# Kernel tuning notes

Measured on AMD Instinct MI355X. Metric: run time of the kernel, lower is better.

The kernel has to match this reference:

```python
import jax, jax.numpy as jnp
import numpy as np

HID = 512
T_CONST = 0.01


def setup_inputs() -> dict:
    key = jax.random.key(0)
    ks = jax.random.split(key, 14)
    B, T, I, H = 32, 1000, 1, HID
    inp = jax.random.normal(ks[0], (B, T, I), jnp.float32)
    hn = jax.random.uniform(ks[1], (1, B, 4 * H), jnp.float32)  # post-relu state, nonneg
    inhib_stim = 0.01 * jax.random.normal(ks[2], (B, T, 4 * H), jnp.float32)
    u = lambda k: jax.random.uniform(k, (H, H), jnp.float32, 0.0, 0.01)
    str2str_w = u(ks[3]); thal2alm_w = u(ks[4]); thal2str_w = u(ks[5])
    alm2alm_w = u(ks[6]); alm2str_w = u(ks[7]); str2snr_w = u(ks[8]); snr2thal_w = u(ks[9])
    inp_weight = jax.random.uniform(ks[10], (I, 4 * H), jnp.float32, 0.0, 0.01)
    sparse_mask = (jax.random.uniform(ks[11], (H, H)) < 0.1).astype(jnp.float32)
    str2str_fixed = jax.random.uniform(ks[12], (H, H), jnp.float32, 0.0, 0.001) * sparse_mask
    return dict(inp=inp, hn=hn, inhib_stim=inhib_stim,
                str2str_w=str2str_w, thal2alm_w=thal2alm_w, thal2str_w=thal2str_w,
                alm2alm_w=alm2alm_w, alm2str_w=alm2str_w, str2snr_w=str2snr_w,
                snr2thal_w=snr2thal_w, inp_weight=inp_weight, str2str_fixed=str2str_fixed)


def reference(inp, hn, inhib_stim, str2str_w, thal2alm_w, thal2str_w,
              alm2alm_w, alm2str_w, str2snr_w, snr2thal_w, inp_weight, str2str_fixed):
    H = str2str_w.shape[0]
    k = int(0.3 * H)  # inhibitory fraction of ALM
    dt = jnp.asarray(T_CONST, inp.dtype)
    ht = lambda w: jnp.clip(w, 1e-15, 1.0)  # F.hardtanh(w, 1e-15, 1)
    Z = jnp.zeros((H, H), inp.dtype)

    # constrained weight blocks (str2str_mask is all zeros, so only the fixed sparse part survives; @ (-I) flips sign)
    str2str = -(0.0 * ht(str2str_w) + str2str_fixed)
    str2snr = -ht(str2snr_w)            # @ (-I)
    snr2thal = -ht(snr2thal_w)          # @ (-I)
    d_alm = jnp.concatenate([jnp.ones(H - k, inp.dtype), -jnp.ones(k, inp.dtype)])
    alm2alm = ht(alm2alm_w) * d_alm[None, :]  # column-scale == @ diag(d_alm)
    alm2str_mask = jnp.concatenate([jnp.ones((H, H - k), inp.dtype), jnp.zeros((H, k), inp.dtype)], axis=1)
    alm2str = alm2str_mask * ht(alm2str_w)
    thal2str_mask = jnp.concatenate([jnp.zeros((H // 2, H), inp.dtype), jnp.ones((H // 2, H), inp.dtype)], axis=0)
    thal2str = thal2str_mask * ht(thal2str_w)
    thal2alm = ht(thal2alm_w)
    iw = ht(inp_weight)

    W_rec = jnp.block([[str2str, Z,        thal2str, alm2str],
                       [str2snr, Z,        Z,        Z      ],
                       [Z,       snr2thal, Z,        Z      ],
                       [Z,       Z,        thal2alm, alm2alm]])  # [4H, 4H]

    strthal_mask = jnp.concatenate([jnp.zeros(H // 2, inp.dtype), jnp.ones(H // 2, inp.dtype),
                                    jnp.zeros(3 * H, inp.dtype)])
    tonic = jnp.concatenate([jnp.zeros(H, inp.dtype), 0.7 * jnp.ones(H, inp.dtype),
                             jnp.ones(H, inp.dtype), jnp.zeros(H, inp.dtype)])

    # precompute time-varying drive (noise=False path): input proj + inhib stim + tonic  [B,T,4H]
    drive = jnp.einsum('bti,ih->bth', inp, iw) * strthal_mask + inhib_stim + tonic

    def step(h, d_t):  # h: [B,4H], d_t: [B,4H]
        h_new = jax.nn.relu(h + dt * (-h + h @ W_rec.T + d_t))
        return h_new, h_new

    h0 = hn[0]  # squeeze(0)
    _, hs = jax.lax.scan(step, h0, jnp.swapaxes(drive, 0, 1))  # hs: [T,B,4H]
    rnn_out = jnp.swapaxes(hs, 0, 1)  # [B,T,4H]
    hn_last = rnn_out[:, -1, :][None]  # [1,B,4H]
    return hn_last, rnn_out
```

## Files before the change

### kernel.cpp

```cpp
#include <hip/hip_runtime.h>
#include <stdint.h>

#define H4T 2048
#define BATCHN 32
#define TSTEPS 1000
#define NBLK 256
#define NTHR 512
#define NSLICE 16
#define WSTRIDE 8192


__device__ __forceinline__ float ht_clip(float w) {
  return fminf(fmaxf(w, 1e-15f), 1.0f);
}

__device__ float wval(int g, int jj, int i,
                      const float* s2s_f, const float* t2s, const float* a2s,
                      const float* s2n, const float* n2t,
                      const float* t2a, const float* a2a) {
  int ig = i >> 9;
  int ii = i & 511;
  float v = 0.0f;
  if (g == 0) {
    if (ig == 0)      v = -s2s_f[jj * 512 + ii];
    else if (ig == 2) v = (jj >= 256) ? ht_clip(t2s[jj * 512 + ii]) : 0.0f;
    else if (ig == 3) v = (ii < 359) ? ht_clip(a2s[jj * 512 + ii]) : 0.0f;
  } else if (g == 1) {
    if (ig == 0)      v = -ht_clip(s2n[jj * 512 + ii]);
  } else if (g == 2) {
    if (ig == 1)      v = -ht_clip(n2t[jj * 512 + ii]);
  } else {
    if (ig == 2)      v = ht_clip(t2a[jj * 512 + ii]);
    else if (ig == 3) v = ht_clip(a2a[jj * 512 + ii]) * ((ii < 359) ? 1.0f : -1.0f);
  }
  return v;
}

__global__ void prep_h0(const float* __restrict__ hn, float* __restrict__ hbuf0) {
  int e = blockIdx.x * blockDim.x + threadIdx.x;
  if (e < BATCHN * H4T) {
    int b = e >> 11;
    int j = e & 2047;
    hbuf0[(j >> 2) * 128 + (b << 2) + (j & 3)] = hn[e];
  }
}

__global__ __launch_bounds__(NTHR) void pack_w(
    const float* s2s_f, const float* t2s, const float* a2s,
    const float* s2n, const float* n2t, const float* t2a, const float* a2a,
    const float* __restrict__ inpw,
    float* __restrict__ wp, float* __restrict__ iwp)
{
  int bid = blockIdx.x, tid = threadIdx.x;
  int g, j0, NC, IE, ib4;
  if (bid < 128)      { g = 0; j0 = bid * 4;              NC = 4;  IE = 1536; ib4 = 0;   }
  else if (bid < 160) { g = 1; j0 = 512 + (bid - 128)*16; NC = 16; IE = 512;  ib4 = 0;   }
  else if (bid < 192) { g = 2; j0 = 1024 + (bid - 160)*16;NC = 16; IE = 512;  ib4 = 128; }
  else                { g = 3; j0 = 1536 + (bid - 192)*8; NC = 8;  IE = 1024; ib4 = 256; }

  for (int idx = tid; idx < NC * IE; idx += NTHR) {
    int c  = idx / IE;
    int fi = idx - c * IE;
    int i  = (g == 0) ? ((fi < 512) ? fi : fi + 512) : ib4 * 4 + fi;
    wp[(size_t)bid * WSTRIDE + idx] =
        wval(g, (j0 + c) & 511, i, s2s_f, t2s, a2s, s2n, n2t, t2a, a2a);
  }
  if (tid < NC) {
    int j = j0 + tid;
    iwp[bid * 16 + tid] = (j >= 256 && j < 512) ? ht_clip(inpw[j]) : 0.0f;
  }
}

template<int NCOLS, int IEXT, bool SPLIT, int LOG2NC>
__device__ __forceinline__ void step_group(
    int j0, int ibase4, float tonicv, int t,
    const float* __restrict__ inp, const float* __restrict__ inhib,
    const float* __restrict__ wp_blk, const float* __restrict__ iwp_blk,
    float* __restrict__ out_hn, float* __restrict__ out_rnn,
    const float* __restrict__ hb, float* __restrict__ hbn,
    float* Wl, float* red, float* outb, float* iwl)
{
  const int tid = threadIdx.x;
  const int b   = tid & 31;
  const int jl  = tid >> 5;
  constexpr int IEXT4  = IEXT / 4;
  constexpr int SLICE4 = IEXT4 / NSLICE;

  {
    const float4* __restrict__ wsrc = (const float4*)wp_blk;
    float4* Wl4w = (float4*)Wl;
    for (int k = tid; k < NCOLS * IEXT4; k += NTHR) Wl4w[k] = wsrc[k];
  }
  if (tid < NCOLS) iwl[tid] = iwp_blk[tid];
  __syncthreads();

  const float dtc = 0.01f;
  const float4* __restrict__ hb4 = (const float4*)hb;
  const float4* __restrict__ Wl4 = (const float4*)Wl;

  float acc[NCOLS];
#pragma unroll
  for (int c = 0; c < NCOLS; ++c) acc[c] = 0.0f;

  for (int it = 0; it < SLICE4; ++it) {
    int fi4 = jl * SLICE4 + it;
    int i4  = ibase4 + (SPLIT ? ((fi4 >= 128) ? fi4 + 128 : fi4) : fi4);
    float4 hv = hb4[i4 * 32 + b];
#pragma unroll
    for (int c = 0; c < NCOLS; ++c) {
      float4 wv = Wl4[c * IEXT4 + fi4];
      acc[c] = fmaf(hv.x, wv.x, acc[c]);
      acc[c] = fmaf(hv.y, wv.y, acc[c]);
      acc[c] = fmaf(hv.z, wv.z, acc[c]);
      acc[c] = fmaf(hv.w, wv.w, acc[c]);
    }
  }

#pragma unroll
  for (int c = 0; c < NCOLS; ++c)
    red[(c * NSLICE + jl) * 33 + b] = acc[c];
  __syncthreads();

  if (tid < 32 * NCOLS) {
    int pb = tid & 31;
    int c  = tid >> 5;
    float s = 0.0f;
#pragma unroll
    for (int sl = 0; sl < NSLICE; ++sl)
      s += red[(c * NSLICE + sl) * 33 + pb];
    int j = j0 + c;
    float hold = hb[(j >> 2) * 128 + (pb << 2) + (j & 3)];
    float inh  = inhib[(size_t)pb * (TSTEPS * H4T) + (size_t)t * H4T + j];
    float iv   = inp[pb * TSTEPS + t];
    float d    = inh + tonicv + iv * iwl[c];
    float hnew = fmaxf(0.0f, fmaf(dtc, s + d - hold, hold));
    hbn[(j >> 2) * 128 + (pb << 2) + (j & 3)] = hnew;
    outb[pb * (NCOLS + 1) + c] = hnew;
  }
  __syncthreads();

  if (tid < 32 * NCOLS) {
    int c  = tid & (NCOLS - 1);
    int bb = tid >> LOG2NC;
    float v = outb[bb * (NCOLS + 1) + c];
    out_rnn[(size_t)bb * (TSTEPS * H4T) + (size_t)t * H4T + (j0 + c)] = v;
    if (t == TSTEPS - 1) out_hn[bb * H4T + (j0 + c)] = v;
  }
}

__global__ __launch_bounds__(NTHR) void rnn_step(
    int t,
    const float* __restrict__ inp, const float* __restrict__ inhib,
    const float* __restrict__ wp, const float* __restrict__ iwp,
    float* __restrict__ out_hn, float* __restrict__ out_rnn,
    const float* __restrict__ hb, float* __restrict__ hbn)
{
  __shared__ __align__(16) float Wl[8192];
  __shared__ float red[8448];
  __shared__ float outb[544];
  __shared__ float iwl[16];

  int bid = blockIdx.x;
  const float* wb = wp + (size_t)bid * WSTRIDE;
  const float* ib = iwp + bid * 16;

  if (bid < 128) {
    step_group<4, 1536, true, 2>(bid * 4, 0, 0.0f, t,
        inp, inhib, wb, ib, out_hn, out_rnn, hb, hbn, Wl, red, outb, iwl);
  } else if (bid < 160) {
    step_group<16, 512, false, 4>(512 + (bid - 128) * 16, 0, 0.7f, t,
        inp, inhib, wb, ib, out_hn, out_rnn, hb, hbn, Wl, red, outb, iwl);
  } else if (bid < 192) {
    step_group<16, 512, false, 4>(1024 + (bid - 160) * 16, 128, 1.0f, t,
        inp, inhib, wb, ib, out_hn, out_rnn, hb, hbn, Wl, red, outb, iwl);
  } else {
    step_group<8, 1024, false, 3>(1536 + (bid - 192) * 8, 256, 0.0f, t,
        inp, inhib, wb, ib, out_hn, out_rnn, hb, hbn, Wl, red, outb, iwl);
  }
}

extern "C" void kernel_launch(void* const* d_in, const int* in_sizes, int n_in,
                              void* d_out, int out_size, void* d_ws, size_t ws_size,
                              hipStream_t stream) {
  const float* inp   = (const float*)d_in[0];
  const float* hn    = (const float*)d_in[1];
  const float* inhib = (const float*)d_in[2];
  const float* t2a   = (const float*)d_in[4];
  const float* t2s   = (const float*)d_in[5];
  const float* a2a   = (const float*)d_in[6];
  const float* a2s   = (const float*)d_in[7];
  const float* s2n   = (const float*)d_in[8];
  const float* n2t   = (const float*)d_in[9];
  const float* inpw  = (const float*)d_in[10];
  const float* s2s_f = (const float*)d_in[11];

  float* out_hn  = (float*)d_out;
  float* out_rnn = out_hn + BATCHN * H4T;

  float* hbuf0 = (float*)d_ws;
  float* hbuf1 = hbuf0 + BATCHN * H4T;
  float* wp    = hbuf1 + BATCHN * H4T;
  float* iwp   = wp + (size_t)NBLK * WSTRIDE;

  prep_h0<<<256, 256, 0, stream>>>(hn, hbuf0);
  pack_w<<<NBLK, NTHR, 0, stream>>>(s2s_f, t2s, a2s, s2n, n2t, t2a, a2a, inpw, wp, iwp);

  for (int t = 0; t < TSTEPS; ++t) {
    const float* hb  = (t & 1) ? hbuf1 : hbuf0;
    float*       hbn = (t & 1) ? hbuf0 : hbuf1;
    rnn_step<<<NBLK, NTHR, 0, stream>>>(t, inp, inhib, wp, iwp,
                                        out_hn, out_rnn, hb, hbn);
  }
}
```

Before: 7.103 ms.

## Read weights directly from global memory and drop LDS staging and output transpose

Each per-timestep block now reads its packed weight slice straight from global memory instead of first copying it into LDS behind a barrier. The reduction buffer is re-indexed so the finalizing threads map column-fastest, letting them write out_rnn directly without the extra outb staging pass and its barrier. This removes one or two __syncthreads and an 8K-float LDS copy per block per step. In exchange, every weight read now goes through L2/L1 cache rather than LDS, and the weight accesses within a wave are broadcast-style loads.

Result: slower. 12.70 ms (+78.9%).

```diff
diff --git a/kernel.cpp b/kernel.cpp
--- a/kernel.cpp
+++ b/kernel.cpp
@@ -78,7 +78,7 @@
     const float* __restrict__ wp_blk, const float* __restrict__ iwp_blk,
     float* __restrict__ out_hn, float* __restrict__ out_rnn,
     const float* __restrict__ hb, float* __restrict__ hbn,
-    float* Wl, float* red, float* outb, float* iwl)
+    float* red)
 {
   const int tid = threadIdx.x;
   const int b   = tid & 31;
@@ -86,29 +86,21 @@
   constexpr int IEXT4  = IEXT / 4;
   constexpr int SLICE4 = IEXT4 / NSLICE;
 
-  {
-    const float4* __restrict__ wsrc = (const float4*)wp_blk;
-    float4* Wl4w = (float4*)Wl;
-    for (int k = tid; k < NCOLS * IEXT4; k += NTHR) Wl4w[k] = wsrc[k];
-  }
-  if (tid < NCOLS) iwl[tid] = iwp_blk[tid];
-  __syncthreads();
-
-  const float dtc = 0.01f;
+  const float4* __restrict__ wp4 = (const float4*)wp_blk;
   const float4* __restrict__ hb4 = (const float4*)hb;
-  const float4* __restrict__ Wl4 = (const float4*)Wl;
 
   float acc[NCOLS];
 #pragma unroll
   for (int c = 0; c < NCOLS; ++c) acc[c] = 0.0f;
 
+#pragma unroll 2
   for (int it = 0; it < SLICE4; ++it) {
     int fi4 = jl * SLICE4 + it;
     int i4  = ibase4 + (SPLIT ? ((fi4 >= 128) ? fi4 + 128 : fi4) : fi4);
     float4 hv = hb4[i4 * 32 + b];
 #pragma unroll
     for (int c = 0; c < NCOLS; ++c) {
-      float4 wv = Wl4[c * IEXT4 + fi4];
+      float4 wv = wp4[c * IEXT4 + fi4];
       acc[c] = fmaf(hv.x, wv.x, acc[c]);
       acc[c] = fmaf(hv.y, wv.y, acc[c]);
       acc[c] = fmaf(hv.z, wv.z, acc[c]);
@@ -118,33 +110,25 @@
 
 #pragma unroll
   for (int c = 0; c < NCOLS; ++c)
-    red[(c * NSLICE + jl) * 33 + b] = acc[c];
+    red[(jl * NCOLS + c) * 33 + b] = acc[c];
   __syncthreads();
 
   if (tid < 32 * NCOLS) {
-    int pb = tid & 31;
-    int c  = tid >> 5;
+    int c  = tid & (NCOLS - 1);
+    int pb = tid >> LOG2NC;
     float s = 0.0f;
 #pragma unroll
     for (int sl = 0; sl < NSLICE; ++sl)
-      s += red[(c * NSLICE + sl) * 33 + pb];
+      s += red[(sl * NCOLS + c) * 33 + pb];
     int j = j0 + c;
     float hold = hb[(j >> 2) * 128 + (pb << 2) + (j & 3)];
     float inh  = inhib[(size_t)pb * (TSTEPS * H4T) + (size_t)t * H4T + j];
     float iv   = inp[pb * TSTEPS + t];
-    float d    = inh + tonicv + iv * iwl[c];
-    float hnew = fmaxf(0.0f, fmaf(dtc, s + d - hold, hold));
+    float d    = inh + tonicv + iv * iwp_blk[c];
+    float hnew = fmaxf(0.0f, fmaf(0.01f, s + d - hold, hold));
     hbn[(j >> 2) * 128 + (pb << 2) + (j & 3)] = hnew;
-    outb[pb * (NCOLS + 1) + c] = hnew;
-  }
-  __syncthreads();
-
-  if (tid < 32 * NCOLS) {
-    int c  = tid & (NCOLS - 1);
-    int bb = tid >> LOG2NC;
-    float v = outb[bb * (NCOLS + 1) + c];
-    out_rnn[(size_t)bb * (TSTEPS * H4T) + (size_t)t * H4T + (j0 + c)] = v;
-    if (t == TSTEPS - 1) out_hn[bb * H4T + (j0 + c)] = v;
+    out_rnn[(size_t)pb * (TSTEPS * H4T) + (size_t)t * H4T + j] = hnew;
+    if (t == TSTEPS - 1) out_hn[pb * H4T + j] = hnew;
   }
 }
 
@@ -155,10 +139,7 @@
     float* __restrict__ out_hn, float* __restrict__ out_rnn,
     const float* __restrict__ hb, float* __restrict__ hbn)
 {
-  __shared__ __align__(16) float Wl[8192];
   __shared__ float red[8448];
-  __shared__ float outb[544];
-  __shared__ float iwl[16];
 
   int bid = blockIdx.x;
   const float* wb = wp + (size_t)bid * WSTRIDE;
@@ -166,16 +147,16 @@
 
   if (bid < 128) {
     step_group<4, 1536, true, 2>(bid * 4, 0, 0.0f, t,
-        inp, inhib, wb, ib, out_hn, out_rnn, hb, hbn, Wl, red, outb, iwl);
+        inp, inhib, wb, ib, out_hn, out_rnn, hb, hbn, red);
   } else if (bid < 160) {
     step_group<16, 512, false, 4>(512 + (bid - 128) * 16, 0, 0.7f, t,
-        inp, inhib, wb, ib, out_hn, out_rnn, hb, hbn, Wl, red, outb, iwl);
+        inp, inhib, wb, ib, out_hn, out_rnn, hb, hbn, red);
   } else if (bid < 192) {
     step_group<16, 512, false, 4>(1024 + (bid - 160) * 16, 128, 1.0f, t,
-        inp, inhib, wb, ib, out_hn, out_rnn, hb, hbn, Wl, red, outb, iwl);
+        inp, inhib, wb, ib, out_hn, out_rnn, hb, hbn, red);
   } else {
     step_group<8, 1024, false, 3>(1536 + (bid - 192) * 8, 256, 0.0f, t,
-        inp, inhib, wb, ib, out_hn, out_rnn, hb, hbn, Wl, red, outb, iwl);
+        inp, inhib, wb, ib, out_hn, out_rnn, hb, hbn, red);
   }
 }
 
```
